# Kernel tuning notes

Measured on AMD Instinct MI355X. Metric: run time of the kernel, lower is better.

The kernel has to match this reference:

```python
import jax, jax.numpy as jnp
from jax import lax
import numpy as np

V, D, H, E, L, B = 512, 128, 64, 4, 60, 4096
ADJ = 184  # ((180 + 7) // 8) * 8


def setup_inputs() -> dict:
    key = jax.random.key(0)
    it = iter(jax.random.split(key, 64))

    def nrm(shape, s=0.05):
        return jax.random.normal(next(it), shape, dtype=jnp.float32) * s

    x = jax.random.randint(next(it), (B, L), 0, V, dtype=jnp.int32)
    inp = {"x": x, "emb": nrm((V, D), 0.02).at[0].set(0.0)}  # padding_idx=0 row zero
    for d in ("f", "r"):
        inp[f"w_ih_{d}"] = nrm((4 * H, D)); inp[f"w_hh_{d}"] = nrm((4 * H, H))
        inp[f"b_ih_{d}"] = nrm((4 * H,)); inp[f"b_hh_{d}"] = nrm((4 * H,))
    for p, i_, h_, o_ in (("e", 1, 16, 8), ("l", 1, 16, 8), ("c", V, 32, 16), ("p", 6, 24, 12), ("x", 4, 16, 8)):
        inp[f"{p}_w1"] = nrm((h_, i_)); inp[f"{p}_b1"] = nrm((h_,))
        inp[f"{p}_w2"] = nrm((o_, h_)); inp[f"{p}_b2"] = nrm((o_,))
    inp["fp_w"] = nrm((ADJ, 180)); inp["fp_b"] = nrm((ADJ,))
    inp["attn_w"] = nrm((3 * ADJ, ADJ)); inp["attn_b"] = nrm((3 * ADJ,))
    inp["out_w"] = nrm((ADJ, ADJ)); inp["out_b"] = nrm((ADJ,))
    for i, (o_, i_) in enumerate(((128, ADJ), (64, 128), (32, 64), (E, 32)), 1):
        inp[f"g_w{i}"] = nrm((o_, i_)); inp[f"g_b{i}"] = nrm((o_,))
    return inp


def _mlp2(h, w1, b1, w2, b2):
    return jnp.maximum(h @ w1.T + b1, 0.0) @ w2.T + b2


def _lstm_final(xe, w_ih, w_hh, b_ih, b_hh):
    # torch LSTM gate order i, f, g, o; returns final hidden state [B, H]
    xg = jnp.einsum('bld,gd->blg', xe, w_ih) + b_ih
    h0 = jnp.zeros((xe.shape[0], H), xe.dtype)

    def step(carry, g_t):
        h, c = carry
        g = g_t + h @ w_hh.T + b_hh
        i, f, gg, o = jnp.split(g, 4, axis=-1)
        c = jax.nn.sigmoid(f) * c + jax.nn.sigmoid(i) * jnp.tanh(gg)
        h = jax.nn.sigmoid(o) * jnp.tanh(c)
        return (h, c), None

    (h, _), _ = lax.scan(step, (h0, h0), jnp.swapaxes(xg, 0, 1))
    return h


def _sequence_stats(x):
    # Fully vectorized equivalent of the per-sequence python loops
    f32 = jnp.float32
    mask = x != 0
    vlen = mask.sum(1)                                       # [B]
    vlenf = jnp.maximum(vlen, 1).astype(f32)
    pos = jnp.arange(L)
    # per-row histogram over valid tokens (torch.bincount of valid_seq)
    counts = jnp.zeros((B, V), f32).at[jnp.arange(B)[:, None], x].add(mask.astype(f32))
    probs = counts / jnp.maximum(counts.sum(1, keepdims=True), 1.0)
    entropy = -jnp.sum(probs * jnp.log(probs + 1e-8), axis=1)
    entropy = jnp.where(vlen > 1, entropy, 0.0)
    char_dist = counts / vlenf[:, None]
    # compact valid tokens to the front (torch: seq[seq != 0]), stable argsort
    order = jnp.argsort((~mask).astype(jnp.int32), axis=1)
    cseq = jnp.take_along_axis(x, order, axis=1)
    cseq = jnp.where(pos[None] < vlen[:, None], cseq, 0)
    a, b = cseq[:, :-1], cseq[:, 1:]
    pairmask = pos[: L - 1][None] < (vlen - 1)[:, None]
    den1 = jnp.maximum(vlen - 1, 1).astype(f32)
    repeat = ((a == b) & pairmask).sum(1) / den1
    inc = ((b > a) & pairmask).sum(1) / den1
    dec = ((b < a) & pairmask).sum(1) / den1
    m2 = pos[: L - 2][None] < (vlen - 2)[:, None]
    per = ((cseq[:, :-2] == cseq[:, 2:]) & m2).sum(1) / jnp.maximum(vlen - 2, 1)
    per = jnp.where(vlen >= 4, per, 0.0)
    diversity = (counts > 0).sum(1) / vlenf
    # longest run of equal consecutive tokens via cummax of reset positions
    eq = jnp.concatenate([jnp.zeros((B, 1), bool), (cseq[:, 1:] == cseq[:, :-1]) & (pos[1:][None] < vlen[:, None])], 1)
    lastreset = lax.cummax(jnp.where(eq, -1, pos[None]), axis=1)
    runlen = pos[None] - lastreset + 1
    max_rep = jnp.where(pos[None] < vlen[:, None], runlen, 0).max(1) / vlenf
    pattern = jnp.stack([repeat, inc, dec, per, diversity, max_rep], 1).astype(f32)
    pattern = jnp.where((vlen > 1)[:, None], pattern, 0.0)
    # unique bigrams: sort pair codes, count distinct valid codes
    codes = jnp.where(pairmask, a * V + b, -1)
    s = jnp.sort(codes, axis=1)
    prevc = jnp.concatenate([jnp.full((B, 1), -2, s.dtype), s[:, :-1]], 1)
    comp_ratio = ((s != prevc) & (s >= 0)).sum(1) / den1
    info_density = entropy / jnp.log(jnp.maximum(vlen, 2).astype(f32))
    # local complexity: mean over sliding windows of (#unique / w), w = min(5, len//2)
    wsel = jnp.minimum(5, vlen // 2)
    local = jnp.zeros((B,), f32)
    for w in (2, 3, 4, 5):
        nwin = L - w + 1
        sh = [cseq[:, k:k + nwin] for k in range(w)]
        u = jnp.ones((B, nwin), f32)
        for k in range(1, w):
            isnew = jnp.ones((B, nwin), bool)
            for m in range(k):
                isnew = isnew & (sh[k] != sh[m])
            u = u + isnew
        winmask = pos[:nwin][None] < (vlen - w + 1)[:, None]
        lc = (u * winmask).sum(1) / w / jnp.maximum(vlen - w + 1, 1)
        local = jnp.where(wsel == w, lc, local)
    trans = 1.0 - repeat  # transitions/(len-1) == 1 - repeat_ratio
    complexity = jnp.stack([comp_ratio, info_density, local, trans], 1).astype(f32)
    complexity = jnp.where((vlen > 1)[:, None], complexity, 0.0)
    return entropy, vlen, char_dist, pattern, complexity


def reference(x, emb, w_ih_f, w_hh_f, b_ih_f, b_hh_f, w_ih_r, w_hh_r, b_ih_r, b_hh_r, e_w1, e_b1, e_w2, e_b2, l_w1, l_b1, l_w2, l_b2, c_w1, c_b1, c_w2, c_b2, p_w1, p_b1, p_w2, p_b2, x_w1, x_b1, x_w2, x_b2, fp_w, fp_b, attn_w, attn_b, out_w, out_b, g_w1, g_b1, g_w2, g_b2, g_w3, g_b3, g_w4, g_b4):
    entropy, vlen, char_dist, pattern, complexity = _sequence_stats(x)
    xe = emb[x]                                               # [B, L, D]
    h_f = _lstm_final(xe, w_ih_f, w_hh_f, b_ih_f, b_hh_f)
    h_r = _lstm_final(xe[:, ::-1], w_ih_r, w_hh_r, b_ih_r, b_hh_r)
    feats = jnp.concatenate([
        h_f, h_r,
        _mlp2((entropy / 4.0)[:, None], e_w1, e_b1, e_w2, e_b2),
        _mlp2((vlen.astype(jnp.float32) / 60.0)[:, None], l_w1, l_b1, l_w2, l_b2),
        _mlp2(char_dist, c_w1, c_b1, c_w2, c_b2),
        _mlp2(pattern, p_w1, p_b1, p_w2, p_b2),
        _mlp2(complexity, x_w1, x_b1, x_w2, x_b2),
    ], axis=1)                                                # [B, 180]
    f = feats @ fp_w.T + fp_b                                 # [B, 184]
    # MultiheadAttention with seq_len == 1: softmax over a single key is 1,
    # so attended = out_proj(v_proj(f)) exactly (q/k projections cancel).
    wv, bv = attn_w[2 * ADJ:], attn_b[2 * ADJ:]
    attended = (f @ wv.T + bv) @ out_w.T + out_b
    h = jnp.maximum(attended @ g_w1.T + g_b1, 0.0)
    h = jnp.maximum(h @ g_w2.T + g_b2, 0.0)
    h = jnp.maximum(h @ g_w3.T + g_b3, 0.0)
    logits = h @ g_w4.T + g_b4
    return jax.nn.softmax(logits, axis=-1)  # eval path (training=False)
```

## Files before the change

### kernel.cpp

```cpp
#include <hip/hip_runtime.h>

#define BATCH 4096
#define SEQL  60
#define VOC   512
#define EMBD  128
#define HID   64
#define GATES 256
#define ADJ   184

typedef __attribute__((ext_vector_type(8))) short short8;
typedef __attribute__((ext_vector_type(4))) float f32x4;
typedef __attribute__((ext_vector_type(4))) unsigned short u16x4;

#define L2E  1.4426950408889634f
#define L2E2 2.8853900817779268f

#define GROW 1040

__device__ __forceinline__ float ex2(float x) {
#if __has_builtin(__builtin_amdgcn_exp2f)
  return __builtin_amdgcn_exp2f(x);
#else
  return exp2f(x);
#endif
}
__device__ __forceinline__ unsigned short f2bf_rne(float f) {
  unsigned int u = __float_as_uint(f);
  unsigned int r = (u + 0x7fffu + ((u >> 16) & 1u)) >> 16;
  return (unsigned short)r;
}
__device__ __forceinline__ unsigned short f2bf(float f) {
  return (unsigned short)((__float_as_uint(f) + 0x8000u) >> 16);
}
__device__ __forceinline__ float dot4(float4 a, float4 b, float acc) {
  acc = fmaf(a.x, b.x, acc); acc = fmaf(a.y, b.y, acc);
  acc = fmaf(a.z, b.z, acc); acc = fmaf(a.w, b.w, acc);
  return acc;
}
__device__ __forceinline__ float wsumf(float v) {
  #pragma unroll
  for (int s = 32; s > 0; s >>= 1) v += __shfl_xor(v, s, 64);
  return v;
}
__device__ __forceinline__ int wsumi(int v) {
  #pragma unroll
  for (int s = 32; s > 0; s >>= 1) v += __shfl_xor(v, s, 64);
  return v;
}
__device__ __forceinline__ int wmaxi(int v) {
  #pragma unroll
  for (int s = 32; s > 0; s >>= 1) v = max(v, __shfl_xor(v, s, 64));
  return v;
}
__device__ __forceinline__ void gload16(const void* g, void* l) {
  __builtin_amdgcn_global_load_lds(
      (const __attribute__((address_space(1))) void*)g,
      (__attribute__((address_space(3))) void*)l, 16, 0, 0);
}

__global__ __launch_bounds__(256) void k_prep(
    const int* __restrict__ x,
    const float* __restrict__ emb,
    const float* __restrict__ wih_f, const float* __restrict__ bif, const float* __restrict__ bhf,
    const float* __restrict__ wih_r, const float* __restrict__ bir, const float* __restrict__ bhr,
    const float* __restrict__ whh_f, const float* __restrict__ whh_r,
    const float* __restrict__ g_w1, const float* __restrict__ g_b1,
    const float* __restrict__ out_w, const float* __restrict__ out_b,
    const float* __restrict__ attn_w, const float* __restrict__ attn_b,
    const float* __restrict__ fp_w, const float* __restrict__ fp_b,
    const float* __restrict__ g_w2, const float* __restrict__ g_w3,
    const float* __restrict__ g_w4, const float* __restrict__ c_w1,
    float* __restrict__ G_f, float* __restrict__ G_r,
    unsigned short* __restrict__ Wfrag,
    float* __restrict__ A, float* __restrict__ avb,
    float* __restrict__ Bp, float* __restrict__ vb,
    float* __restrict__ g_w2t, float* __restrict__ g_w3t, float* __restrict__ g_w4t,
    float* __restrict__ c_w1t,
    float* __restrict__ ent_o, float* __restrict__ vlen_o,
    float* __restrict__ pat_o, float* __restrict__ cpx_o) {
  __shared__ unsigned int cnt[4][512];
  __shared__ unsigned short q[4][68];
  const int bid = blockIdx.x;
  const int tid = threadIdx.x;

  if (bid < 128) {
    const int dir = bid >> 6;
    const int rem = bid & 63;
    const int v0 = (rem >> 2) * 32;
    const int j0 = (rem & 3) * 64;
    const float* W = dir ? wih_r : wih_f;
    const float* bi = dir ? bir : bif;
    const float* bh = dir ? bhr : bhf;
    float* G = dir ? G_r : G_f;
    const int vp = tid >> 4;
    const int jq = tid & 15;
    const int v = v0 + vp * 2;
    const int j = j0 + jq * 4;
    const int gg = j >> 6;
    const int u0 = j & 63;
    const float sc = (gg == 2) ? L2E2 : L2E;

    const float4* E0 = (const float4*)(emb + (size_t)v * 128);
    const float4* E1 = (const float4*)(emb + (size_t)(v + 1) * 128);
    const float4* W0 = (const float4*)(W + (size_t)j * 128);
    const float4* W1 = (const float4*)(W + (size_t)(j + 1) * 128);
    const float4* W2 = (const float4*)(W + (size_t)(j + 2) * 128);
    const float4* W3 = (const float4*)(W + (size_t)(j + 3) * 128);

    float a00 = 0.f, a01 = 0.f, a02 = 0.f, a03 = 0.f;
    float a10 = 0.f, a11 = 0.f, a12 = 0.f, a13 = 0.f;
    #pragma unroll 4
    for (int d4 = 0; d4 < 32; d4++) {
      float4 e0 = E0[d4], e1 = E1[d4];
      float4 w0 = W0[d4], w1 = W1[d4], w2 = W2[d4], w3 = W3[d4];
      a00 = dot4(e0, w0, a00); a01 = dot4(e0, w1, a01);
      a02 = dot4(e0, w2, a02); a03 = dot4(e0, w3, a03);
      a10 = dot4(e1, w0, a10); a11 = dot4(e1, w1, a11);
      a12 = dot4(e1, w2, a12); a13 = dot4(e1, w3, a13);
    }
    float b0v = bi[j] + bh[j], b1v = bi[j + 1] + bh[j + 1];
    float b2v = bi[j + 2] + bh[j + 2], b3v = bi[j + 3] + bh[j + 3];
    float* g0 = G + (size_t)v * 256 + u0 * 4 + gg;
    g0[0]  = (a00 + b0v) * sc; g0[4]  = (a01 + b1v) * sc;
    g0[8]  = (a02 + b2v) * sc; g0[12] = (a03 + b3v) * sc;
    float* g1 = g0 + 256;
    g1[0]  = (a10 + b0v) * sc; g1[4]  = (a11 + b1v) * sc;
    g1[8]  = (a12 + b2v) * sc; g1[12] = (a13 + b3v) * sc;
  } else if (bid < 144) {
    const int id = (bid - 128) * 256 + tid;
    const int lane = id & 63;
    const int fc = id >> 6;
    const int c = fc & 1;
    const int gg = (fc >> 1) & 3;
    const int w = (fc >> 3) & 3;
    const int dir = fc >> 5;
    const float* whh = dir ? whh_r : whh_f;
    const float sc = (gg == 2) ? L2E2 : L2E;
    const int n = gg * 64 + w * 16 + (lane & 15);
    const int kb = c * 32 + (lane >> 4) * 8;
    unsigned short* o = Wfrag + (size_t)id * 8;
    #pragma unroll
    for (int j = 0; j < 8; j++) o[j] = f2bf_rne(whh[n * 64 + kb + j] * sc);
  } else if (bid < 272) {
    const int i = bid - 144;
    const int j = tid;
    const float* g1r = g_w1 + (size_t)i * ADJ;
    if (j < ADJ) {
      float a0 = 0.f, a1 = 0.f, a2 = 0.f, a3 = 0.f;
      for (int k = 0; k < ADJ; k += 4) {
        a0 = fmaf(g1r[k],     out_w[(size_t)(k)     * ADJ + j], a0);
        a1 = fmaf(g1r[k + 1], out_w[(size_t)(k + 1) * ADJ + j], a1);
        a2 = fmaf(g1r[k + 2], out_w[(size_t)(k + 2) * ADJ + j], a2);
        a3 = fmaf(g1r[k + 3], out_w[(size_t)(k + 3) * ADJ + j], a3);
      }
      A[(size_t)i * ADJ + j] = (a0 + a1) + (a2 + a3);
    } else if (j == ADJ) {
      float a0 = 0.f;
      for (int k = 0; k < ADJ; k++) a0 = fmaf(g1r[k], out_b[k], a0);
      avb[i] = a0 + g_b1[i];
    }
  } else if (bid < 456) {
    const int k = bid - 272;
    const int j = tid;
    const float* wvr = attn_w + (size_t)(2 * ADJ + k) * ADJ;
    if (j < 180) {
      float a0 = 0.f, a1 = 0.f, a2 = 0.f, a3 = 0.f;
      for (int m = 0; m < ADJ; m += 4) {
        a0 = fmaf(wvr[m],     fp_w[(size_t)(m)     * 180 + j], a0);
        a1 = fmaf(wvr[m + 1], fp_w[(size_t)(m + 1) * 180 + j], a1);
        a2 = fmaf(wvr[m + 2], fp_w[(size_t)(m + 2) * 180 + j], a2);
        a3 = fmaf(wvr[m + 3], fp_w[(size_t)(m + 3) * 180 + j], a3);
      }
      Bp[(size_t)k * 180 + j] = (a0 + a1) + (a2 + a3);
    } else if (j == 180) {
      float a0 = 0.f;
      for (int m = 0; m < ADJ; m++) a0 = fmaf(wvr[m], fp_b[m], a0);
      vb[k] = a0 + attn_b[2 * ADJ + k];
    }
  } else if (bid == 456) {
    for (int i = tid; i < 64 * 128; i += 256) {
      int o = i >> 7, k = i & 127;
      g_w2t[k * 64 + o] = g_w2[i];
    }
    for (int i = tid; i < 32 * 64; i += 256) {
      int o = i >> 6, k = i & 63;
      g_w3t[k * 32 + o] = g_w3[i];
    }
    if (tid < 128) {
      int o = tid >> 5, k = tid & 31;
      g_w4t[k * 4 + o] = g_w4[tid];
    }
  } else if (bid < 465) {
    const int base = (bid - 457) * 2048;
    for (int i = tid; i < 2048; i += 256) {
      int idx = base + i;
      int o = idx >> 9, k = idx & 511;
      c_w1t[k * 32 + o] = k ? c_w1[o * 512 + k] : 0.f;
    }
  } else {
    const int lane = tid & 63;
    const int wid = tid >> 6;
    const int row = (bid - 465) * 4 + wid;
    unsigned int* cr = cnt[wid];
    unsigned short* qr = q[wid];

    for (int i = lane; i < 512; i += 64) cr[i] = 0u;
    qr[lane] = 0;
    if (lane < 4) qr[64 + lane] = 0;
    int v = (lane < 60) ? x[row * 60 + lane] : 0;
    bool act = (v != 0);
    unsigned long long amask = __ballot(act);
    int n = __popcll(amask);
    __syncthreads();
    if (act) {
      int pos = __popcll(amask & ((1ull << lane) - 1ull));
      qr[pos] = (unsigned short)v;
      atomicAdd(&cr[v], 1u);
    }
    __syncthreads();

    float vlenf = (float)(n >= 1 ? n : 1);
    float inv = 1.f / vlenf;

    float ent = 0.f; int distinct = 0;
    #pragma unroll
    for (int j = 0; j < 8; j++) {
      unsigned int c = cr[lane + j * 64];
      if (c) {
        distinct++;
        float p = (float)c * inv;
        ent -= p * __logf(p + 1e-8f);
      }
    }
    ent = wsumf(ent);
    distinct = wsumi(distinct);

    int a = qr[lane], b = qr[lane + 1], c2 = qr[lane + 2];
    bool v1 = (lane + 1 < n);
    bool v2 = (lane + 2 < n);
    int rep  = __popcll(__ballot(v1 && (a == b)));
    int incs = __popcll(__ballot(v1 && (b > a)));
    int decs = __popcll(__ballot(v1 && (b < a)));
    int per2 = __popcll(__ballot(v2 && (a == c2)));

    int prev = (lane > 0) ? (int)qr[lane - 1] : -1;
    bool isst = (lane < n) && (lane == 0 || a != prev);
    unsigned long long smask = __ballot(isst);
    int len = 0;
    if (isst) {
      unsigned long long hi = (lane < 63) ? (smask >> (lane + 1)) : 0ull;
      int next = hi ? (lane + __ffsll((unsigned long long)hi)) : n;
      len = next - lane;
    }
    int maxrun = wmaxi(len);

    int code = v1 ? (a * VOC + b) : -1;
    int unique = v1 ? 1 : 0;
    #pragma unroll 1
    for (int j = 0; j < 58; j++) {
      int cj = __shfl(code, j, 64);
      if (j < lane && cj == code) unique = 0;
    }
    int dc = __popcll(__ballot(unique != 0));

    int wl = n >> 1; if (wl > 5) wl = 5;
    float local = 0.f;
    if (wl >= 2) {
      bool pv = (lane + wl <= n);
      int u = 0;
      if (pv) {
        int t0 = qr[lane], t1 = qr[lane + 1], t2 = qr[lane + 2];
        int t3 = qr[lane + 3], t4 = qr[lane + 4];
        u = 1;
        u += (t1 != t0);
        if (wl >= 3) u += (int)((t2 != t1) && (t2 != t0));
        if (wl >= 4) u += (int)((t3 != t2) && (t3 != t1) && (t3 != t0));
        if (wl >= 5) u += (int)((t4 != t3) && (t4 != t2) && (t4 != t1) && (t4 != t0));
      }
      int usum = wsumi(u);
      int denw = n - wl + 1; if (denw < 1) denw = 1;
      local = (float)usum / (float)wl / (float)denw;
    }

    float den1 = (float)((n - 1) >= 1 ? (n - 1) : 1);
    float repeat = (float)rep / den1;
    float per = (n >= 4) ? (float)per2 / (float)((n - 2) >= 1 ? (n - 2) : 1) : 0.f;
    float entz = (n > 1) ? ent : 0.f;
    float z = (n > 1) ? 1.f : 0.f;

    if (lane == 0) {
      ent_o[row] = entz;
      vlen_o[row] = (float)n;
      pat_o[row * 6 + 0] = repeat * z;
      pat_o[row * 6 + 1] = (float)incs / den1 * z;
      pat_o[row * 6 + 2] = (float)decs / den1 * z;
      pat_o[row * 6 + 3] = per * z;
      pat_o[row * 6 + 4] = (float)distinct * inv * z;
      pat_o[row * 6 + 5] = (float)maxrun * inv * z;
      cpx_o[row * 4 + 0] = (float)dc / den1 * z;
      cpx_o[row * 4 + 1] = entz / __logf((float)(n >= 2 ? n : 2)) * z;
      cpx_o[row * 4 + 2] = local * z;
      cpx_o[row * 4 + 3] = (1.f - repeat) * z;
    }
  }
}

#define LSTM_STEP(T)                                                           \
  {                                                                            \
    if ((T) < 59) {                                                            \
      const int tsn = dir ? (58 - (T)) : ((T) + 1);                            \
      const unsigned int* toks = tokoff + tsn * 16;                            \
      char* gdst = Gm + (((T) + 1) & 1) * (16 * GROW) + r4 * GROW;             \
      gload16(GbC + toks[r4 + 0] + lane16, gdst);                              \
      gload16(GbC + toks[r4 + 1] + lane16, gdst + GROW);                       \
      gload16(GbC + toks[r4 + 2] + lane16, gdst + 2 * GROW);                   \
      gload16(GbC + toks[r4 + 3] + lane16, gdst + 3 * GROW);                   \
    }                                                                          \
    const unsigned short* hb = hbuf[(T) & 1];                                  \
    short8 hf0 = *(const short8*)(hb + rdoff);                                 \
    short8 hf1 = *(const short8*)(hb + rdoff + 32);                            \
    const char* gbp = Gm + ((T) & 1) * (16 * GROW) + goff;                     \
    float4 gvv[4];                                                             \
    gvv[0] = *(const float4*)(gbp);                                            \
    gvv[1] = *(const float4*)(gbp + 16);                                       \
    gvv[2] = *(const float4*)(gbp + 32);                                       \
    gvv[3] = *(const float4*)(gbp + 48);                                       \
    f32x4 z0 = {0.f, 0.f, 0.f, 0.f};                                           \
    f32x4 acc0 = z0, acc1 = z0, acc2 = z0, acc3 = z0;                          \
    acc0 = __builtin_amdgcn_mfma_f32_16x16x32_bf16(bfr[0][0], hf0, acc0, 0, 0, 0); \
    acc1 = __builtin_amdgcn_mfma_f32_16x16x32_bf16(bfr[1][0], hf0, acc1, 0, 0, 0); \
    acc2 = __builtin_amdgcn_mfma_f32_16x16x32_bf16(bfr[2][0], hf0, acc2, 0, 0, 0); \
    acc3 = __builtin_amdgcn_mfma_f32_16x16x32_bf16(bfr[3][0], hf0, acc3, 0, 0, 0); \
    acc0 = __builtin_amdgcn_mfma_f32_16x16x32_bf16(bfr[0][1], hf1, acc0, 0, 0, 0); \
    acc1 = __builtin_amdgcn_mfma_f32_16x16x32_bf16(bfr[1][1], hf1, acc1, 0, 0, 0); \
    acc2 = __builtin_amdgcn_mfma_f32_16x16x32_bf16(bfr[2][1], hf1, acc2, 0, 0, 0); \
    acc3 = __builtin_amdgcn_mfma_f32_16x16x32_bf16(bfr[3][1], hf1, acc3, 0, 0, 0); \
    unsigned short* hw = hbuf[((T) + 1) & 1];                                  \
    unsigned short hh[4];                                                      \
    float hv[4];                                                               \
    _Pragma("unroll")                                                          \
    for (int r = 0; r < 4; r++) {                                              \
      float gi = acc0[r] + gvv[r].x;                                           \
      float gf = acc1[r] + gvv[r].y;                                           \
      float gc = acc2[r] + gvv[r].z;                                           \
      float go = acc3[r] + gvv[r].w;                                           \
      float Ef = ex2(-gf);                                                     \
      float E1 = ex2(-gi);                                                     \
      float E2 = ex2(gc);                                                      \
      float sf = __builtin_amdgcn_rcpf(1.f + Ef);                              \
      float p  = (E2 - 1.f) * __builtin_amdgcn_rcpf((1.f + E1) * (E2 + 1.f));  \
      float cn = fmaf(sf, cst[r], p);                                          \
      cst[r] = cn;                                                             \
      float E3 = ex2(-go);                                                     \
      float E4 = ex2(fminf(L2E2 * cn, 126.f));                                 \
      float h  = (E4 - 1.f) * __builtin_amdgcn_rcpf((1.f + E3) * (E4 + 1.f));  \
      hv[r] = h;                                                               \
      hh[r] = f2bf(h);                                                         \
    }                                                                          \
    u16x4 hvv = {hh[0], hh[1], hh[2], hh[3]};                                  \
    *(u16x4*)(hw + wroff) = hvv;                                               \
    if ((T) == 59) {                                                           \
      float4 o4; o4.x = hv[0]; o4.y = hv[1]; o4.z = hv[2]; o4.w = hv[3];       \
      *(float4*)(hop) = o4;                                                    \
    }                                                                          \
    __syncthreads();                                                           \
  }

__global__ __launch_bounds__(256) void k_main(
    const int* __restrict__ x,
    const float* __restrict__ G_f, const float* __restrict__ G_r,
    const unsigned short* __restrict__ Wfrag,
    const float* __restrict__ A, const float* __restrict__ avb,
    const float* __restrict__ Bp, const float* __restrict__ vb,
    float* __restrict__ C1t, float* __restrict__ c1b,
    float* __restrict__ hf_o, float* __restrict__ hr_o) {
  __shared__ __align__(16) char Gm[2 * 16 * GROW];
  __shared__ __align__(16) unsigned short hbuf[2][16 * 72];
  __shared__ __align__(16) unsigned int tokoff[60 * 16];
  const int bid = blockIdx.x;
  const int tid = threadIdx.x;

  if (bid < 512) {
    const int lane = tid & 63;
    const int w = tid >> 6;
    const int dir = bid >> 8;
    const int blk = bid & 255;
    const int b0 = blk << 4;
    const float* G = dir ? G_r : G_f;
    const char* GbC = (const char*)G;
    float* ho = dir ? hr_o : hf_o;

    for (int i = tid; i < 960; i += 256) {
      int r = i / 60, t = i - r * 60;
      tokoff[t * 16 + r] = ((unsigned int)x[(size_t)(b0 + r) * 60 + t]) << 10;
    }
    for (int i = tid; i < 16 * 72; i += 256) hbuf[0][i] = 0;

    short8 bfr[4][2];
    #pragma unroll
    for (int gg = 0; gg < 4; gg++)
      #pragma unroll
      for (int c = 0; c < 2; c++) {
        int idx = (((dir * 4 + w) * 4 + gg) * 2 + c) * 64 + lane;
        bfr[gg][c] = *(const short8*)(Wfrag + (size_t)idx * 8);
      }

    const int kg = lane >> 4;
    const int ln = lane & 15;
    const int ub2 = w * 16 + kg * 4;
    const int rdoff = ln * 72 + kg * 8;
    const int wroff = ln * 72 + ub2;
    const int r4 = w * 4;
    const int lane16 = lane * 16;
    const int goff = ln * GROW + ub2 * 16;
    float* hop = ho + (size_t)(b0 + ln) * 64 + ub2;
    float cst[4] = {0.f, 0.f, 0.f, 0.f};

    __syncthreads();

    {
      const int ts0 = dir ? 59 : 0;
      const unsigned int* toks = tokoff + ts0 * 16;
      char* gdst = Gm + r4 * GROW;
      gload16(GbC + toks[r4 + 0] + lane16, gdst);
      gload16(GbC + toks[r4 + 1] + lane16, gdst + GROW);
      gload16(GbC + toks[r4 + 2] + lane16, gdst + 2 * GROW);
      gload16(GbC + toks[r4 + 3] + lane16, gdst + 3 * GROW);
    }
    __syncthreads();

    #pragma unroll 1
    for (int tt = 0; tt < 30; tt++) {
      const int t0 = tt * 2, t1 = tt * 2 + 1;
      LSTM_STEP(t0)
      LSTM_STEP(t1)
    }
  } else {
    const int i = bid - 512, j = tid;
    const float* Ar = A + (size_t)i * ADJ;
    if (j < 180) {
      float a0 = 0.f, a1 = 0.f, a2 = 0.f, a3 = 0.f;
      for (int k = 0; k < ADJ; k += 4) {
        a0 = fmaf(Ar[k],     Bp[(size_t)(k)     * 180 + j], a0);
        a1 = fmaf(Ar[k + 1], Bp[(size_t)(k + 1) * 180 + j], a1);
        a2 = fmaf(Ar[k + 2], Bp[(size_t)(k + 2) * 180 + j], a2);
        a3 = fmaf(Ar[k + 3], Bp[(size_t)(k + 3) * 180 + j], a3);
      }
      C1t[(size_t)j * 128 + i] = (a0 + a1) + (a2 + a3);
    } else if (j == 180) {
      float a0 = 0.f;
      for (int k = 0; k < ADJ; k++) a0 = fmaf(Ar[k], vb[k], a0);
      c1b[i] = a0 + avb[i];
    }
  }
}

#define FSTR 192

__global__ __launch_bounds__(256) void k_head(
    const int* __restrict__ x,
    const float* __restrict__ hf, const float* __restrict__ hr,
    const float* __restrict__ ent, const float* __restrict__ vlen,
    const float* __restrict__ pat, const float* __restrict__ cpx,
    const float* __restrict__ e_w1, const float* __restrict__ e_b1,
    const float* __restrict__ e_w2, const float* __restrict__ e_b2,
    const float* __restrict__ l_w1, const float* __restrict__ l_b1,
    const float* __restrict__ l_w2, const float* __restrict__ l_b2,
    const float* __restrict__ c_w1t, const float* __restrict__ c_b1,
    const float* __restrict__ c_w2, const float* __restrict__ c_b2,
    const float* __restrict__ p_w1, const float* __restrict__ p_b1,
    const float* __restrict__ p_w2, const float* __restrict__ p_b2,
    const float* __restrict__ x_w1, const float* __restrict__ x_b1,
    const float* __restrict__ x_w2, const float* __restrict__ x_b2,
    const float* __restrict__ C1t, const float* __restrict__ c1b,
    const float* __restrict__ g_w2t, const float* __restrict__ g_b2,
    const float* __restrict__ g_w3t, const float* __restrict__ g_b3,
    const float* __restrict__ g_w4t, const float* __restrict__ g_b4,
    float* __restrict__ out) {
  __shared__ float feat[8 * FSTR];
  __shared__ unsigned short tk[8 * 64];
  __shared__ float h1[8 * 128];
  __shared__ float h2[8 * 64];
  __shared__ float h3[8 * 32];
  __shared__ float h1c[8 * 33];
  __shared__ float lg[32];
  const int tid = threadIdx.x;
  const int b0 = blockIdx.x * 8;

  if (tid < 128) {
    int r = tid >> 4, c = tid & 15;
    float4 vv = ((const float4*)(hf + (size_t)(b0 + r) * 64))[c];
    *(float4*)(feat + r * FSTR + c * 4) = vv;
  } else {
    int t = tid - 128;
    int r = t >> 4, c = t & 15;
    float4 vv = ((const float4*)(hr + (size_t)(b0 + r) * 64))[c];
    *(float4*)(feat + r * FSTR + 64 + c * 4) = vv;
  }
  for (int i = tid; i < 480; i += 256) {
    int r = i / 60, t = i - r * 60;
    tk[r * 64 + t] = (unsigned short)x[(size_t)(b0 + r) * 60 + t];
  }
  __syncthreads();
  {
    int o = tid & 31, r = tid >> 5;
    const unsigned short* tkr = tk + r * 64;
    float a0 = 0.f, a1 = 0.f, a2 = 0.f, a3 = 0.f;
    #pragma unroll 5
    for (int t = 0; t < 60; t += 4) {
      int t0 = tkr[t], t1 = tkr[t + 1], t2 = tkr[t + 2], t3 = tkr[t + 3];
      a0 += c_w1t[t0 * 32 + o];
      a1 += c_w1t[t1 * 32 + o];
      a2 += c_w1t[t2 * 32 + o];
      a3 += c_w1t[t3 * 32 + o];
    }
    float invv = __builtin_amdgcn_rcpf(fmaxf(vlen[b0 + r], 1.f));
    h1c[r * 33 + o] = fmaxf(((a0 + a1) + (a2 + a3)) * invv + c_b1[o], 0.f);
  }
  __syncthreads();
  if (tid < 32) {
    const int m = tid & 3, r = tid >> 2, b = b0 + r;
    float tt[24];
    if (m == 0) {
      float ein = ent[b] * 0.25f;
      #pragma unroll
      for (int o = 0; o < 16; o++) tt[o] = fmaxf(e_w1[o] * ein + e_b1[o], 0.f);
      #pragma unroll
      for (int o = 0; o < 8; o++) {
        float a = e_b2[o];
        #pragma unroll
        for (int k = 0; k < 16; k++) a = fmaf(e_w2[o * 16 + k], tt[k], a);
        feat[r * FSTR + 128 + o] = a;
      }
    } else if (m == 1) {
      float lin = vlen[b] * (1.f / 60.f);
      #pragma unroll
      for (int o = 0; o < 16; o++) tt[o] = fmaxf(l_w1[o] * lin + l_b1[o], 0.f);
      #pragma unroll
      for (int o = 0; o < 8; o++) {
        float a = l_b2[o];
        #pragma unroll
        for (int k = 0; k < 16; k++) a = fmaf(l_w2[o * 16 + k], tt[k], a);
        feat[r * FSTR + 136 + o] = a;
      }
    } else if (m == 2) {
      float pin[6];
      #pragma unroll
      for (int k = 0; k < 6; k++) pin[k] = pat[b * 6 + k];
      #pragma unroll
      for (int o = 0; o < 24; o++) {
        float a = p_b1[o];
        #pragma unroll
        for (int k = 0; k < 6; k++) a = fmaf(p_w1[o * 6 + k], pin[k], a);
        tt[o] = fmaxf(a, 0.f);
      }
      #pragma unroll
      for (int o = 0; o < 12; o++) {
        float a = p_b2[o];
        #pragma unroll
        for (int k = 0; k < 24; k++) a = fmaf(p_w2[o * 24 + k], tt[k], a);
        feat[r * FSTR + 160 + o] = a;
      }
    } else {
      float xin[4];
      #pragma unroll
      for (int k = 0; k < 4; k++) xin[k] = cpx[b * 4 + k];
      #pragma unroll
      for (int o = 0; o < 16; o++) {
        float a = x_b1[o];
        #pragma unroll
        for (int k = 0; k < 4; k++) a = fmaf(x_w1[o * 4 + k], xin[k], a);
        tt[o] = fmaxf(a, 0.f);
      }
      #pragma unroll
      for (int o = 0; o < 8; o++) {
        float a = x_b2[o];
        #pragma unroll
        for (int k = 0; k < 16; k++) a = fmaf(x_w2[o * 16 + k], tt[k], a);
        feat[r * FSTR + 172 + o] = a;
      }
    }
  } else if (tid >= 64 && tid < 192) {
    int t = tid - 64;
    int r = t >> 4, o = t & 15;
    float a = c_b2[o];
    const float* hh = h1c + r * 33;
    #pragma unroll
    for (int k = 0; k < 32; k++) a = fmaf(c_w2[o * 32 + k], hh[k], a);
    feat[r * FSTR + 144 + o] = a;
  }
  __syncthreads();

  {
    const int o = tid & 127, rg = tid >> 7;
    const float* f0p = feat + (rg * 4 + 0) * FSTR;
    const float* f1p = feat + (rg * 4 + 1) * FSTR;
    const float* f2p = feat + (rg * 4 + 2) * FSTR;
    const float* f3p = feat + (rg * 4 + 3) * FSTR;
    float a0 = 0.f, a1 = 0.f, a2 = 0.f, a3 = 0.f;
    #pragma unroll 3
    for (int k4 = 0; k4 < 45; k4++) {
      float w0 = C1t[(size_t)(k4 * 4 + 0) * 128 + o];
      float w1 = C1t[(size_t)(k4 * 4 + 1) * 128 + o];
      float w2 = C1t[(size_t)(k4 * 4 + 2) * 128 + o];
      float w3 = C1t[(size_t)(k4 * 4 + 3) * 128 + o];
      float4 f0 = *(const float4*)(f0p + k4 * 4);
      float4 f1 = *(const float4*)(f1p + k4 * 4);
      float4 f2 = *(const float4*)(f2p + k4 * 4);
      float4 f3 = *(const float4*)(f3p + k4 * 4);
      a0 = fmaf(w0, f0.x, a0); a0 = fmaf(w1, f0.y, a0);
      a0 = fmaf(w2, f0.z, a0); a0 = fmaf(w3, f0.w, a0);
      a1 = fmaf(w0, f1.x, a1); a1 = fmaf(w1, f1.y, a1);
      a1 = fmaf(w2, f1.z, a1); a1 = fmaf(w3, f1.w, a1);
      a2 = fmaf(w0, f2.x, a2); a2 = fmaf(w1, f2.y, a2);
      a2 = fmaf(w2, f2.z, a2); a2 = fmaf(w3, f2.w, a2);
      a3 = fmaf(w0, f3.x, a3); a3 = fmaf(w1, f3.y, a3);
      a3 = fmaf(w2, f3.z, a3); a3 = fmaf(w3, f3.w, a3);
    }
    float bb = c1b[o];
    h1[(rg * 4 + 0) * 128 + o] = fmaxf(a0 + bb, 0.f);
    h1[(rg * 4 + 1) * 128 + o] = fmaxf(a1 + bb, 0.f);
    h1[(rg * 4 + 2) * 128 + o] = fmaxf(a2 + bb, 0.f);
    h1[(rg * 4 + 3) * 128 + o] = fmaxf(a3 + bb, 0.f);
  }
  __syncthreads();
  {
    const int o = tid & 63, rg = tid >> 6;
    const float* f0p = h1 + (rg * 2 + 0) * 128;
    const float* f1p = h1 + (rg * 2 + 1) * 128;
    float a0 = 0.f, a1 = 0.f;
    #pragma unroll 4
    for (int k4 = 0; k4 < 32; k4++) {
      float w0 = g_w2t[(k4 * 4 + 0) * 64 + o];
      float w1 = g_w2t[(k4 * 4 + 1) * 64 + o];
      float w2 = g_w2t[(k4 * 4 + 2) * 64 + o];
      float w3 = g_w2t[(k4 * 4 + 3) * 64 + o];
      float4 f0 = *(const float4*)(f0p + k4 * 4);
      float4 f1 = *(const float4*)(f1p + k4 * 4);
      a0 = fmaf(w0, f0.x, a0); a0 = fmaf(w1, f0.y, a0);
      a0 = fmaf(w2, f0.z, a0); a0 = fmaf(w3, f0.w, a0);
      a1 = fmaf(w0, f1.x, a1); a1 = fmaf(w1, f1.y, a1);
      a1 = fmaf(w2, f1.z, a1); a1 = fmaf(w3, f1.w, a1);
    }
    float bb = g_b2[o];
    h2[(rg * 2 + 0) * 64 + o] = fmaxf(a0 + bb, 0.f);
    h2[(rg * 2 + 1) * 64 + o] = fmaxf(a1 + bb, 0.f);
  }
  __syncthreads();
  {
    const int o = tid & 31, rg = tid >> 5;
    const float* fp = h2 + rg * 64;
    float a = 0.f;
    #pragma unroll 4
    for (int k4 = 0; k4 < 16; k4++) {
      float w0 = g_w3t[(k4 * 4 + 0) * 32 + o];
      float w1 = g_w3t[(k4 * 4 + 1) * 32 + o];
      float w2 = g_w3t[(k4 * 4 + 2) * 32 + o];
      float w3 = g_w3t[(k4 * 4 + 3) * 32 + o];
      float4 f0 = *(const float4*)(fp + k4 * 4);
      a = fmaf(w0, f0.x, a); a = fmaf(w1, f0.y, a);
      a = fmaf(w2, f0.z, a); a = fmaf(w3, f0.w, a);
    }
    h3[rg * 32 + o] = fmaxf(a + g_b3[o], 0.f);
  }
  __syncthreads();
  if (tid < 32) {
    int r = tid >> 2, o = tid & 3;
    const float* hh = h3 + r * 32;
    float a = g_b4[o];
    #pragma unroll
    for (int k = 0; k < 32; k++) a = fmaf(g_w4t[k * 4 + o], hh[k], a);
    lg[tid] = a;
  }
  __syncthreads();
  if (tid < 8) {
    float l0 = lg[tid * 4 + 0], l1 = lg[tid * 4 + 1];
    float l2 = lg[tid * 4 + 2], l3 = lg[tid * 4 + 3];
    float m = fmaxf(fmaxf(l0, l1), fmaxf(l2, l3));
    float e0 = __expf(l0 - m), e1 = __expf(l1 - m);
    float e2 = __expf(l2 - m), e3 = __expf(l3 - m);
    float is = __builtin_amdgcn_rcpf(e0 + e1 + e2 + e3);
    float4 o4; o4.x = e0 * is; o4.y = e1 * is; o4.z = e2 * is; o4.w = e3 * is;
    *(float4*)(out + (size_t)(b0 + tid) * 4) = o4;
  }
}

extern "C" void kernel_launch(void* const* d_in, const int* in_sizes, int n_in,
                              void* d_out, int out_size, void* d_ws, size_t ws_size,
                              hipStream_t stream) {
  const int*   x     = (const int*)d_in[0];
  const float* emb   = (const float*)d_in[1];
  const float* wih_f = (const float*)d_in[2];
  const float* whh_f = (const float*)d_in[3];
  const float* bih_f = (const float*)d_in[4];
  const float* bhh_f = (const float*)d_in[5];
  const float* wih_r = (const float*)d_in[6];
  const float* whh_r = (const float*)d_in[7];
  const float* bih_r = (const float*)d_in[8];
  const float* bhh_r = (const float*)d_in[9];
  const float* e_w1 = (const float*)d_in[10]; const float* e_b1 = (const float*)d_in[11];
  const float* e_w2 = (const float*)d_in[12]; const float* e_b2 = (const float*)d_in[13];
  const float* l_w1 = (const float*)d_in[14]; const float* l_b1 = (const float*)d_in[15];
  const float* l_w2 = (const float*)d_in[16]; const float* l_b2 = (const float*)d_in[17];
  const float* c_w1 = (const float*)d_in[18]; const float* c_b1 = (const float*)d_in[19];
  const float* c_w2 = (const float*)d_in[20]; const float* c_b2 = (const float*)d_in[21];
  const float* p_w1 = (const float*)d_in[22]; const float* p_b1 = (const float*)d_in[23];
  const float* p_w2 = (const float*)d_in[24]; const float* p_b2 = (const float*)d_in[25];
  const float* x_w1 = (const float*)d_in[26]; const float* x_b1 = (const float*)d_in[27];
  const float* x_w2 = (const float*)d_in[28]; const float* x_b2 = (const float*)d_in[29];
  const float* fp_w = (const float*)d_in[30]; const float* fp_b = (const float*)d_in[31];
  const float* attn_w = (const float*)d_in[32]; const float* attn_b = (const float*)d_in[33];
  const float* out_w = (const float*)d_in[34]; const float* out_b = (const float*)d_in[35];
  const float* g_w1 = (const float*)d_in[36]; const float* g_b1 = (const float*)d_in[37];
  const float* g_w2 = (const float*)d_in[38]; const float* g_b2 = (const float*)d_in[39];
  const float* g_w3 = (const float*)d_in[40]; const float* g_b3 = (const float*)d_in[41];
  const float* g_w4 = (const float*)d_in[42]; const float* g_b4 = (const float*)d_in[43];

  float* ws   = (float*)d_ws;
  float* G_f  = ws;
  float* G_r  = G_f  + 512 * 256;
  float* hfw  = G_r  + 512 * 256;
  float* hrw  = hfw  + BATCH * 64;
  float* entw = hrw  + BATCH * 64;
  float* vlnw = entw + BATCH;
  float* patw = vlnw + BATCH;
  float* cpxw = patw + BATCH * 6;
  float* Aw   = cpxw + BATCH * 4;
  float* avbw = Aw + 128 * ADJ;
  float* Bpw  = avbw + 128;
  float* vbw  = Bpw + ADJ * 180;
  float* C1t  = vbw + ADJ;
  float* c1b  = C1t + 180 * 128;
  float* g2t  = c1b + 128;
  float* g3t  = g2t + 128 * 64;
  float* g4t  = g3t + 64 * 32;
  float* cw1t = g4t + 32 * 4;
  unsigned short* Wfrag = (unsigned short*)(cw1t + 512 * 32);

  k_prep<<<dim3(465 + BATCH / 4), dim3(256), 0, stream>>>(
      x, emb, wih_f, bih_f, bhh_f, wih_r, bih_r, bhh_r, whh_f, whh_r,
      g_w1, g_b1, out_w, out_b, attn_w, attn_b, fp_w, fp_b,
      g_w2, g_w3, g_w4, c_w1,
      G_f, G_r, Wfrag, Aw, avbw, Bpw, vbw, g2t, g3t, g4t, cw1t,
      entw, vlnw, patw, cpxw);
  k_main<<<dim3(640), dim3(256), 0, stream>>>(
      x, G_f, G_r, Wfrag, Aw, avbw, Bpw, vbw, C1t, c1b, hfw, hrw);
  k_head<<<dim3(BATCH / 8), dim3(256), 0, stream>>>(
      x, hfw, hrw, entw, vlnw, patw, cpxw,
      e_w1, e_b1, e_w2, e_b2, l_w1, l_b1, l_w2, l_b2,
      cw1t, c_b1, c_w2, c_b2, p_w1, p_b1, p_w2, p_b2,
      x_w1, x_b1, x_w2, x_b2, C1t, c1b,
      g2t, g_b2, g3t, g_b3, g4t, g_b4,
      (float*)d_out);
}
```

Baseline: 246.2 us.

## Split LSTM recurrence across eight waves with gate-interleaved MFMA weight fragments

The LSTM recurrence block grows from 4 to 8 waves, so each wave now computes 2 hidden units per row instead of 4. The recurrent-weight fragments are re-laid out so that one 16x16 MFMA output tile holds the i, f, g and o gates of the same unit together. Each wave then issues 4 MFMAs, runs half the transcendental work and makes half the G-row loads per timestep. This shortens the serial per-step critical path of the latency-bound scan. The cost is a block-wide barrier across twice as many waves and idle extra threads in the non-LSTM blocks of the same kernel.

```diff
diff --git a/kernel.cpp b/kernel.cpp
--- a/kernel.cpp
+++ b/kernel.cpp
@@ -10,7 +10,6 @@
 
 typedef __attribute__((ext_vector_type(8))) short short8;
 typedef __attribute__((ext_vector_type(4))) float f32x4;
-typedef __attribute__((ext_vector_type(4))) unsigned short u16x4;
 
 #define L2E  1.4426950408889634f
 #define L2E2 2.8853900817779268f
@@ -131,12 +130,16 @@
     const int lane = id & 63;
     const int fc = id >> 6;
     const int c = fc & 1;
-    const int gg = (fc >> 1) & 3;
-    const int w = (fc >> 3) & 3;
+    const int hh = (fc >> 1) & 1;
+    const int w = (fc >> 2) & 7;
     const int dir = fc >> 5;
     const float* whh = dir ? whh_r : whh_f;
-    const float sc = (gg == 2) ? L2E2 : L2E;
-    const int n = gg * 64 + w * 16 + (lane & 15);
+    const int rr = lane & 15;
+    const int du = rr >> 2;
+    const int gate = rr & 3;
+    const int unit = w * 8 + hh * 4 + du;
+    const float sc = (gate == 2) ? L2E2 : L2E;
+    const int n = gate * 64 + unit;
     const int kb = c * 32 + (lane >> 4) * 8;
     unsigned short* o = Wfrag + (size_t)id * 8;
     #pragma unroll
@@ -310,63 +313,66 @@
     if ((T) < 59) {                                                            \
       const int tsn = dir ? (58 - (T)) : ((T) + 1);                            \
       const unsigned int* toks = tokoff + tsn * 16;                            \
-      char* gdst = Gm + (((T) + 1) & 1) * (16 * GROW) + r4 * GROW;             \
-      gload16(GbC + toks[r4 + 0] + lane16, gdst);                              \
-      gload16(GbC + toks[r4 + 1] + lane16, gdst + GROW);                       \
-      gload16(GbC + toks[r4 + 2] + lane16, gdst + 2 * GROW);                   \
-      gload16(GbC + toks[r4 + 3] + lane16, gdst + 3 * GROW);                   \
+      char* gdst = Gm + (((T) + 1) & 1) * (16 * GROW) + r2 * GROW;             \
+      gload16(GbC + toks[r2 + 0] + lane16, gdst);                              \
+      gload16(GbC + toks[r2 + 1] + lane16, gdst + GROW);                       \
     }                                                                          \
     const unsigned short* hb = hbuf[(T) & 1];                                  \
     short8 hf0 = *(const short8*)(hb + rdoff);                                 \
     short8 hf1 = *(const short8*)(hb + rdoff + 32);                            \
     const char* gbp = Gm + ((T) & 1) * (16 * GROW) + goff;                     \
-    float4 gvv[4];                                                             \
-    gvv[0] = *(const float4*)(gbp);                                            \
-    gvv[1] = *(const float4*)(gbp + 16);                                       \
-    gvv[2] = *(const float4*)(gbp + 32);                                       \
-    gvv[3] = *(const float4*)(gbp + 48);                                       \
+    float4 gv0 = *(const float4*)(gbp);                                        \
+    float4 gv1 = *(const float4*)(gbp + 64);                                   \
     f32x4 z0 = {0.f, 0.f, 0.f, 0.f};                                           \
-    f32x4 acc0 = z0, acc1 = z0, acc2 = z0, acc3 = z0;                          \
+    f32x4 acc0 = z0, acc1 = z0;                                                \
     acc0 = __builtin_amdgcn_mfma_f32_16x16x32_bf16(bfr[0][0], hf0, acc0, 0, 0, 0); \
     acc1 = __builtin_amdgcn_mfma_f32_16x16x32_bf16(bfr[1][0], hf0, acc1, 0, 0, 0); \
-    acc2 = __builtin_amdgcn_mfma_f32_16x16x32_bf16(bfr[2][0], hf0, acc2, 0, 0, 0); \
-    acc3 = __builtin_amdgcn_mfma_f32_16x16x32_bf16(bfr[3][0], hf0, acc3, 0, 0, 0); \
     acc0 = __builtin_amdgcn_mfma_f32_16x16x32_bf16(bfr[0][1], hf1, acc0, 0, 0, 0); \
     acc1 = __builtin_amdgcn_mfma_f32_16x16x32_bf16(bfr[1][1], hf1, acc1, 0, 0, 0); \
-    acc2 = __builtin_amdgcn_mfma_f32_16x16x32_bf16(bfr[2][1], hf1, acc2, 0, 0, 0); \
-    acc3 = __builtin_amdgcn_mfma_f32_16x16x32_bf16(bfr[3][1], hf1, acc3, 0, 0, 0); \
     unsigned short* hw = hbuf[((T) + 1) & 1];                                  \
-    unsigned short hh[4];                                                      \
-    float hv[4];                                                               \
-    _Pragma("unroll")                                                          \
-    for (int r = 0; r < 4; r++) {                                              \
-      float gi = acc0[r] + gvv[r].x;                                           \
-      float gf = acc1[r] + gvv[r].y;                                           \
-      float gc = acc2[r] + gvv[r].z;                                           \
-      float go = acc3[r] + gvv[r].w;                                           \
+    float h0, h1;                                                              \
+    {                                                                          \
+      float gi = acc0[0] + gv0.x;                                              \
+      float gf = acc0[1] + gv0.y;                                              \
+      float gc = acc0[2] + gv0.z;                                              \
+      float go = acc0[3] + gv0.w;                                              \
       float Ef = ex2(-gf);                                                     \
       float E1 = ex2(-gi);                                                     \
       float E2 = ex2(gc);                                                      \
       float sf = __builtin_amdgcn_rcpf(1.f + Ef);                              \
       float p  = (E2 - 1.f) * __builtin_amdgcn_rcpf((1.f + E1) * (E2 + 1.f));  \
-      float cn = fmaf(sf, cst[r], p);                                          \
-      cst[r] = cn;                                                             \
+      float cn = fmaf(sf, cst0, p);                                            \
+      cst0 = cn;                                                               \
       float E3 = ex2(-go);                                                     \
       float E4 = ex2(fminf(L2E2 * cn, 126.f));                                 \
-      float h  = (E4 - 1.f) * __builtin_amdgcn_rcpf((1.f + E3) * (E4 + 1.f));  \
-      hv[r] = h;                                                               \
-      hh[r] = f2bf(h);                                                         \
+      h0 = (E4 - 1.f) * __builtin_amdgcn_rcpf((1.f + E3) * (E4 + 1.f));        \
     }                                                                          \
-    u16x4 hvv = {hh[0], hh[1], hh[2], hh[3]};                                  \
-    *(u16x4*)(hw + wroff) = hvv;                                               \
+    {                                                                          \
+      float gi = acc1[0] + gv1.x;                                              \
+      float gf = acc1[1] + gv1.y;                                              \
+      float gc = acc1[2] + gv1.z;                                              \
+      float go = acc1[3] + gv1.w;                                              \
+      float Ef = ex2(-gf);                                                     \
+      float E1 = ex2(-gi);                                                     \
+      float E2 = ex2(gc);                                                      \
+      float sf = __builtin_amdgcn_rcpf(1.f + Ef);                              \
+      float p  = (E2 - 1.f) * __builtin_amdgcn_rcpf((1.f + E1) * (E2 + 1.f));  \
+      float cn = fmaf(sf, cst1, p);                                            \
+      cst1 = cn;                                                               \
+      float E3 = ex2(-go);                                                     \
+      float E4 = ex2(fminf(L2E2 * cn, 126.f));                                 \
+      h1 = (E4 - 1.f) * __builtin_amdgcn_rcpf((1.f + E3) * (E4 + 1.f));        \
+    }                                                                          \
+    hw[wr0] = f2bf(h0);                                                        \
+    hw[wr0 + 4] = f2bf(h1);                                                    \
     if ((T) == 59) {                                                           \
-      float4 o4; o4.x = hv[0]; o4.y = hv[1]; o4.z = hv[2]; o4.w = hv[3];       \
-      *(float4*)(hop) = o4;                                                    \
+      hop[0] = h0;                                                             \
+      hop[4] = h1;                                                             \
     }                                                                          \
     __syncthreads();                                                           \
   }
 
-__global__ __launch_bounds__(256) void k_main(
+__global__ __launch_bounds__(512) void k_main(
     const int* __restrict__ x,
     const float* __restrict__ G_f, const float* __restrict__ G_r,
     const unsigned short* __restrict__ Wfrag,
@@ -390,42 +396,40 @@
     const char* GbC = (const char*)G;
     float* ho = dir ? hr_o : hf_o;
 
-    for (int i = tid; i < 960; i += 256) {
+    for (int i = tid; i < 960; i += 512) {
       int r = i / 60, t = i - r * 60;
       tokoff[t * 16 + r] = ((unsigned int)x[(size_t)(b0 + r) * 60 + t]) << 10;
     }
-    for (int i = tid; i < 16 * 72; i += 256) hbuf[0][i] = 0;
-
-    short8 bfr[4][2];
+    for (int i = tid; i < 16 * 72; i += 512) hbuf[0][i] = 0;
+
+    short8 bfr[2][2];
     #pragma unroll
-    for (int gg = 0; gg < 4; gg++)
+    for (int hh = 0; hh < 2; hh++)
       #pragma unroll
       for (int c = 0; c < 2; c++) {
-        int idx = (((dir * 4 + w) * 4 + gg) * 2 + c) * 64 + lane;
-        bfr[gg][c] = *(const short8*)(Wfrag + (size_t)idx * 8);
+        int idx = (((dir * 8 + w) * 2 + hh) * 2 + c) * 64 + lane;
+        bfr[hh][c] = *(const short8*)(Wfrag + (size_t)idx * 8);
       }
 
     const int kg = lane >> 4;
     const int ln = lane & 15;
-    const int ub2 = w * 16 + kg * 4;
+    const int u0 = w * 8 + kg;
     const int rdoff = ln * 72 + kg * 8;
-    const int wroff = ln * 72 + ub2;
-    const int r4 = w * 4;
+    const int wr0 = ln * 72 + u0;
+    const int r2 = w * 2;
     const int lane16 = lane * 16;
-    const int goff = ln * GROW + ub2 * 16;
-    float* hop = ho + (size_t)(b0 + ln) * 64 + ub2;
-    float cst[4] = {0.f, 0.f, 0.f, 0.f};
+    const int goff = ln * GROW + u0 * 16;
+    float* hop = ho + (size_t)(b0 + ln) * 64 + u0;
+    float cst0 = 0.f, cst1 = 0.f;
 
     __syncthreads();
 
     {
       const int ts0 = dir ? 59 : 0;
       const unsigned int* toks = tokoff + ts0 * 16;
-      char* gdst = Gm + r4 * GROW;
-      gload16(GbC + toks[r4 + 0] + lane16, gdst);
-      gload16(GbC + toks[r4 + 1] + lane16, gdst + GROW);
-      gload16(GbC + toks[r4 + 2] + lane16, gdst + 2 * GROW);
-      gload16(GbC + toks[r4 + 3] + lane16, gdst + 3 * GROW);
+      char* gdst = Gm + r2 * GROW;
+      gload16(GbC + toks[r2 + 0] + lane16, gdst);
+      gload16(GbC + toks[r2 + 1] + lane16, gdst + GROW);
     }
     __syncthreads();
 
@@ -743,7 +747,7 @@
       g_w2, g_w3, g_w4, c_w1,
       G_f, G_r, Wfrag, Aw, avbw, Bpw, vbw, g2t, g3t, g4t, cw1t,
       entw, vlnw, patw, cpxw);
-  k_main<<<dim3(640), dim3(256), 0, stream>>>(
+  k_main<<<dim3(640), dim3(512), 0, stream>>>(
       x, G_f, G_r, Wfrag, Aw, avbw, Bpw, vbw, C1t, c1b, hfw, hrw);
   k_head<<<dim3(BATCH / 8), dim3(256), 0, stream>>>(
       x, hfw, hrw, entw, vlnw, patw, cpxw,
```

Result: no change. 243.7 us (-1.0%).
